# Kernel optimization log

Measured on AMD Instinct MI355X. Metric: run time of the kernel, lower is better.

## Reference

```python
import jax, jax.numpy as jnp
import numpy as np

DIM = 1024
NUM_HEADS = 16
HEAD_DIM = DIM // NUM_HEADS
WINDOW = 128
EPS = 1e-5


def setup_inputs() -> dict:
    key = jax.random.key(0)
    ks = jax.random.split(key, 8)
    B, S, D = 1, 2048, DIM
    x = jax.random.normal(ks[0], (B, S, D), dtype=jnp.float32)
    # xavier-uniform-ish scale for linear weights (torch layout: [out, in])
    def xavier(k, out_f, in_f):
        lim = np.sqrt(6.0 / (in_f + out_f)).astype(np.float32)
        return jax.random.uniform(k, (out_f, in_f), jnp.float32, -lim, lim)
    qkv_w = xavier(ks[1], 3 * D, D)
    out_w = xavier(ks[2], D, D)
    ln_g = jnp.ones((D,), jnp.float32)
    ln_b = jnp.zeros((D,), jnp.float32)
    w1 = xavier(ks[3], 4 * D, D)
    b1 = jnp.zeros((4 * D,), jnp.float32)
    w2 = xavier(ks[4], D, 4 * D)
    b2 = jnp.zeros((D,), jnp.float32)
    return {"x": x, "qkv_w": qkv_w, "out_w": out_w, "ln_g": ln_g,
            "ln_b": ln_b, "w1": w1, "b1": b1, "w2": w2, "b2": b2}


def reference(x, qkv_w, out_w, ln_g, ln_b, w1, b1, w2, b2):
    B, S, D = x.shape
    H, hd = NUM_HEADS, HEAD_DIM
    residual = x
    # LayerNorm (pre-norm)
    mu = jnp.mean(x, axis=-1, keepdims=True)
    var = jnp.var(x, axis=-1, keepdims=True)
    xn = (x - mu) * jax.lax.rsqrt(var + EPS) * ln_g + ln_b
    # QKV projection (torch Linear: y = x @ W^T)
    qkv = xn @ qkv_w.T                              # [B,S,3D]
    qkv = qkv.reshape(B, S, 3, H, hd).transpose(2, 0, 3, 1, 4)  # [3,B,H,S,hd]
    q, k, v = qkv[0], qkv[1], qkv[2]
    # Local-window boolean mask: |i - j| <= window_size // 2
    w = WINDOW // 2
    i = jnp.arange(S)[:, None]
    j = jnp.arange(S)[None, :]
    local_mask = jnp.abs(i - j) <= w                # [S,S]
    # SDPA with boolean mask
    scale = 1.0 / np.sqrt(hd).astype(np.float32)
    scores = jnp.einsum('bhqd,bhkd->bhqk', q, k) * scale
    scores = jnp.where(local_mask, scores, -jnp.inf)
    attn = jax.nn.softmax(scores, axis=-1)
    attn_out = jnp.einsum('bhqk,bhkd->bhqd', attn, v)
    attn_out = attn_out.transpose(0, 2, 1, 3).reshape(B, S, D)
    attn_out = attn_out @ out_w.T
    out = residual + attn_out
    # FFN (no second norm in this module), exact GELU
    h = jax.nn.gelu(out @ w1.T + b1, approximate=False)
    ffn_out = h @ w2.T + b2
    return out + ffn_out
```

## Files before the change

kernel.cpp:

```cpp
#include <hip/hip_runtime.h>
#include <math.h>

typedef unsigned short u16;
typedef __attribute__((ext_vector_type(8))) short short8;
typedef __attribute__((ext_vector_type(4))) float f32x4;
typedef __attribute__((ext_vector_type(4))) int i32x4;
typedef __attribute__((ext_vector_type(4))) u16 u16x4;

#define AS1 __attribute__((address_space(1)))
#define AS3 __attribute__((address_space(3)))

__device__ inline u16 f2bf(float f){
  union { float f; unsigned int u; } x; x.f = f;
  unsigned int r = x.u + 0x7fffu + ((x.u >> 16) & 1u);
  return (u16)(r >> 16);
}
__device__ inline float bf2f(u16 u){
  union { unsigned int u; float f; } x; x.u = ((unsigned int)u) << 16;
  return x.f;
}
__device__ inline float gelu_fast(float v){
  float y = 0.7978845608f * (v + 0.044715f * v * v * v);
  float e = __expf(2.0f * y);
  return v - v / (e + 1.0f);
}

__global__ __launch_bounds__(256) void prep_kernel(
    const float* __restrict__ x, const float* __restrict__ g, const float* __restrict__ b,
    u16* __restrict__ xn,
    const float* __restrict__ qkv_w, u16* __restrict__ qkvw_b,
    const float* __restrict__ out_w, u16* __restrict__ outw_b,
    const float* __restrict__ w1,    u16* __restrict__ w1_b,
    const float* __restrict__ w2,    u16* __restrict__ w2_b)
{
  const int tid = threadIdx.x;
  int bid = blockIdx.x;
  if (bid < 2048){
    const int row = bid;
    float4 v = *(const float4*)(x + (size_t)row*1024 + tid*4);
    float s  = v.x + v.y + v.z + v.w;
    float ss = v.x*v.x + v.y*v.y + v.z*v.z + v.w*v.w;
    #pragma unroll
    for (int off = 32; off; off >>= 1){
      s  += __shfl_xor(s,  off, 64);
      ss += __shfl_xor(ss, off, 64);
    }
    __shared__ float red[8];
    const int wid = tid >> 6;
    if ((tid & 63) == 0){ red[wid] = s; red[4+wid] = ss; }
    __syncthreads();
    float S  = red[0]+red[1]+red[2]+red[3];
    float SS = red[4]+red[5]+red[6]+red[7];
    float mu  = S * (1.0f/1024.0f);
    float var = SS * (1.0f/1024.0f) - mu*mu;
    float rs  = rsqrtf(var + 1e-5f);
    float4 gv = *(const float4*)(g + tid*4);
    float4 bv = *(const float4*)(b + tid*4);
    u16x4 pk;
    pk.x = f2bf((v.x-mu)*rs*gv.x + bv.x);
    pk.y = f2bf((v.y-mu)*rs*gv.y + bv.y);
    pk.z = f2bf((v.z-mu)*rs*gv.z + bv.z);
    pk.w = f2bf((v.w-mu)*rs*gv.w + bv.w);
    *(u16x4*)(xn + (size_t)row*1024 + tid*4) = pk;
    return;
  }
  bid -= 2048;
  const float* src; u16* dst;
  if (bid < 3072){ src = qkv_w; dst = qkvw_b; }
  else if (bid < 3072+1024){ src = out_w; dst = outw_b; bid -= 3072; }
  else if (bid < 3072+1024+4096){ src = w1; dst = w1_b; bid -= 3072+1024; }
  else { src = w2; dst = w2_b; bid -= 3072+1024+4096; }
  const size_t i = ((size_t)bid*256 + tid) * 4;
  float4 v = *(const float4*)(src + i);
  u16x4 pk;
  pk.x = f2bf(v.x); pk.y = f2bf(v.y); pk.z = f2bf(v.z); pk.w = f2bf(v.w);
  *(u16x4*)(dst + i) = pk;
}

template<int EPI, int BM, int BN, int WAVES>
__global__ __launch_bounds__(WAVES*64) void gemm_lds(
    const u16* __restrict__ A, const u16* __restrict__ B,
    float* __restrict__ outF, u16* __restrict__ outB,
    const float* __restrict__ bias, const float* __restrict__ resid,
    int M, int N, int K, int nbx, int nwg, int Kc)
{
  constexpr int WR  = (WAVES == 8) ? 4 : 2;
  constexpr int WC  = 2;
  constexpr int MI  = BM / WR / 16;
  constexpr int NJ  = BN / WC / 16;
  constexpr int ACH = BM / 8 / WAVES;
  constexpr int BCH = BN / 8 / WAVES;
  __shared__ u16 As[2][BM*64];
  __shared__ u16 Bs[2][BN*64];
  const int tid = threadIdx.x;
  const int l   = tid & 63;
  const int w   = tid >> 6;
  const int wr  = w & (WR-1), wc = w / WR;
  const int orig = blockIdx.x;
  const int wgid = (orig & 7) * (nwg >> 3) + (orig >> 3);
  const int bcol = wgid % nbx, brow = wgid / nbx;
  const int kz = blockIdx.y;
  const int l15 = l & 15, l4 = l >> 4;

  const u16* Ab = A + (size_t)brow*BM*K + (size_t)kz*Kc;
  const u16* Bb = B + (size_t)bcol*BN*K + (size_t)kz*Kc;

  f32x4 acc[MI][NJ];
  #pragma unroll
  for (int i = 0; i < MI; ++i)
    #pragma unroll
    for (int j = 0; j < NJ; ++j)
      acc[i][j] = (f32x4){0.f, 0.f, 0.f, 0.f};

  const int rsub = l >> 3;
  const int csrc = ((l & 7) ^ rsub) * 8;
  const int swz  = (l15 & 7) * 8;
  const int nkt = Kc >> 6;

  auto stage = [&](int kt, int buf){
    const u16* Ag = Ab + kt*64 + csrc;
    const u16* Bg = Bb + kt*64 + csrc;
    #pragma unroll
    for (int i = 0; i < ACH; ++i){
      const int ca = w*ACH + i;
      __builtin_amdgcn_global_load_lds(
        (const AS1 void*)(Ag + (size_t)(ca*8 + rsub)*K),
        (AS3 void*)(&As[buf][ca*512]), 16, 0, 0);
    }
    #pragma unroll
    for (int i = 0; i < BCH; ++i){
      const int cb = w*BCH + i;
      __builtin_amdgcn_global_load_lds(
        (const AS1 void*)(Bg + (size_t)(cb*8 + rsub)*K),
        (AS3 void*)(&Bs[buf][cb*512]), 16, 0, 0);
    }
  };

  stage(0, 0);
  __syncthreads();
  for (int kt = 0; kt < nkt; ++kt){
    const int cur = kt & 1;
    if (kt + 1 < nkt) stage(kt + 1, cur ^ 1);
    #pragma unroll
    for (int ks = 0; ks < 2; ++ks){
      const int kop = (ks*32 + l4*8) ^ swz;
      short8 af[MI], bfr[NJ];
      #pragma unroll
      for (int i = 0; i < MI; ++i)
        af[i]  = *(const short8*)&As[cur][(wr*(BM/WR) + i*16 + l15)*64 + kop];
      #pragma unroll
      for (int j = 0; j < NJ; ++j)
        bfr[j] = *(const short8*)&Bs[cur][(wc*(BN/WC) + j*16 + l15)*64 + kop];
      #pragma unroll
      for (int i = 0; i < MI; ++i)
        #pragma unroll
        for (int j = 0; j < NJ; ++j)
          acc[i][j] = __builtin_amdgcn_mfma_f32_16x16x32_bf16(af[i], bfr[j], acc[i][j], 0, 0, 0);
    }
    __syncthreads();
  }

  #pragma unroll
  for (int i = 0; i < MI; ++i){
    #pragma unroll
    for (int j = 0; j < NJ; ++j){
      #pragma unroll
      for (int r = 0; r < 4; ++r){
        int row = brow*BM + wr*(BM/WR) + i*16 + l4*4 + r;
        int col = bcol*BN + wc*(BN/WC) + j*16 + l15;
        float v = acc[i][j][r];
        size_t o = (size_t)row * N + col;
        if constexpr (EPI == 0){
          outB[o] = f2bf(v);
        } else if constexpr (EPI == 1){
          v += resid[o];
          outB[o] = f2bf(v);
        } else if constexpr (EPI == 2){
          v += bias[col];
          outB[o] = f2bf(gelu_fast(v));
        } else {
          outB[(size_t)kz * M * N + o] = f2bf(v);
        }
      }
    }
  }
}

__global__ __launch_bounds__(256) void reduce_ffn2(const u16* __restrict__ p,
                                                   const float* __restrict__ bias,
                                                   const u16* __restrict__ resid_b,
                                                   float* __restrict__ out){
  const size_t s = (size_t)2048*1024;
  const size_t i = ((size_t)blockIdx.x * 256 + threadIdx.x) * 4;
  u16x4 a0 = *(const u16x4*)(p + i);
  u16x4 a1 = *(const u16x4*)(p + s + i);
  u16x4 a2 = *(const u16x4*)(p + 2*s + i);
  u16x4 a3 = *(const u16x4*)(p + 3*s + i);
  u16x4 rb = *(const u16x4*)(resid_b + i);
  float4 bb = *(const float4*)(bias + (i & 1023));
  float4 o;
  o.x = bf2f(a0.x) + bf2f(a1.x) + bf2f(a2.x) + bf2f(a3.x) + bf2f(rb.x) + bb.x;
  o.y = bf2f(a0.y) + bf2f(a1.y) + bf2f(a2.y) + bf2f(a3.y) + bf2f(rb.y) + bb.y;
  o.z = bf2f(a0.z) + bf2f(a1.z) + bf2f(a2.z) + bf2f(a3.z) + bf2f(rb.z) + bb.z;
  o.w = bf2f(a0.w) + bf2f(a1.w) + bf2f(a2.w) + bf2f(a3.w) + bf2f(rb.w) + bb.w;
  *(float4*)(out + i) = o;
}

__global__ __launch_bounds__(256) void attn_kernel(const u16* __restrict__ qkv, u16* __restrict__ attn_out){
  constexpr int S = 2048, D3 = 3072;
  const int qt = blockIdx.x, h = blockIdx.y;
  const int q0 = qt * 64;
  const int tid = threadIdx.x;
  const int l = tid & 63, w = tid >> 6;
  const int l15 = l & 15, l4 = l >> 4;

  __shared__ u16 smem[29696];
  u16 (*Qs)[72]  = (u16(*)[72]) (smem);
  u16 *Ks        = smem + 4608;
  u16 (*Ps)[200] = (u16(*)[200])(smem);
  u16 (*Vt)[200] = (u16(*)[200])(smem + 16896);

  #pragma unroll
  for (int i = 0; i < 2; ++i){
    int cid = tid + 256*i; int r = cid >> 3, c = cid & 7;
    *(i32x4*)&Qs[r][c*8] = *(const i32x4*)(qkv + (size_t)(q0 + r)*D3 + h*64 + c*8);
  }
  {
    const int rsubK = l >> 3;
    const int csrcK = ((l & 7) ^ rsubK) * 8;
    #pragma unroll
    for (int i = 0; i < 6; ++i){
      const int ca = w*6 + i;
      const long kj = (long)(q0 - 64 + ca*8 + rsubK);
      __builtin_amdgcn_global_load_lds(
        (const AS1 void*)(qkv + kj*D3 + 1024 + h*64 + csrcK),
        (AS3 void*)(Ks + ca*512), 16, 0, 0);
    }
  }
  #pragma unroll
  for (int i = 0; i < 6; ++i){
    int cid = tid + 256*i; int r = cid >> 3, c = cid & 7;
    int kj = q0 - 64 + r;
    i32x4 vv = {0,0,0,0};
    if (kj >= 0 && kj < S)
      vv = *(const i32x4*)(qkv + (size_t)kj*D3 + 2048 + h*64 + c*8);
    union { i32x4 v; u16 u[8]; } uu; uu.v = vv;
    #pragma unroll
    for (int j = 0; j < 8; ++j) Vt[c*8 + j][r] = uu.u[j];
  }
  __syncthreads();

  f32x4 sc[12];
  #pragma unroll
  for (int cf = 0; cf < 12; ++cf) sc[cf] = (f32x4){0.f,0.f,0.f,0.f};
  const int ko = l4 * 8;
  const int swzK = (l15 & 7) * 8;
  short8 a0 = *(const short8*)&Qs[16*w + l15][ko];
  short8 a1 = *(const short8*)&Qs[16*w + l15][32 + ko];
  #pragma unroll
  for (int cf = 0; cf < 12; ++cf){
    short8 b0 = *(const short8*)&Ks[(cf*16 + l15)*64 + (ko ^ swzK)];
    short8 b1 = *(const short8*)&Ks[(cf*16 + l15)*64 + ((32 + ko) ^ swzK)];
    sc[cf] = __builtin_amdgcn_mfma_f32_16x16x32_bf16(a0, b0, sc[cf], 0, 0, 0);
    sc[cf] = __builtin_amdgcn_mfma_f32_16x16x32_bf16(a1, b1, sc[cf], 0, 0, 0);
  }
  __syncthreads();

  const float scale = 0.125f;
  #pragma unroll
  for (int r = 0; r < 4; ++r){
    const int qrl = 16*w + l4*4 + r;
    float mx = -1e30f;
    #pragma unroll
    for (int cf = 0; cf < 12; ++cf){
      int j  = cf*16 + l15;
      int kj = q0 - 64 + j;
      bool ok = (j >= qrl) && (j <= qrl + 128) && (kj >= 0) && (kj < S);
      float sv = ok ? sc[cf][r]*scale : -1e30f;
      sc[cf][r] = sv;
      mx = fmaxf(mx, sv);
    }
    #pragma unroll
    for (int off = 1; off < 16; off <<= 1) mx = fmaxf(mx, __shfl_xor(mx, off, 64));
    float sm = 0.f;
    #pragma unroll
    for (int cf = 0; cf < 12; ++cf){
      float pv = __expf(sc[cf][r] - mx);
      sc[cf][r] = pv;
      sm += pv;
    }
    #pragma unroll
    for (int off = 1; off < 16; off <<= 1) sm += __shfl_xor(sm, off, 64);
    float inv = 1.0f / sm;
    #pragma unroll
    for (int cf = 0; cf < 12; ++cf) Ps[qrl][cf*16 + l15] = f2bf(sc[cf][r] * inv);
  }
  __syncthreads();

  f32x4 o[4];
  #pragma unroll
  for (int df = 0; df < 4; ++df) o[df] = (f32x4){0.f,0.f,0.f,0.f};
  #pragma unroll
  for (int kk = 0; kk < 6; ++kk){
    short8 a = *(const short8*)&Ps[16*w + l15][kk*32 + ko];
    #pragma unroll
    for (int df = 0; df < 4; ++df){
      short8 b = *(const short8*)&Vt[df*16 + l15][kk*32 + ko];
      o[df] = __builtin_amdgcn_mfma_f32_16x16x32_bf16(a, b, o[df], 0, 0, 0);
    }
  }
  #pragma unroll
  for (int df = 0; df < 4; ++df){
    #pragma unroll
    for (int r = 0; r < 4; ++r){
      attn_out[(size_t)(q0 + 16*w + l4*4 + r)*1024 + h*64 + df*16 + l15] = f2bf(o[df][r]);
    }
  }
}

extern "C" void kernel_launch(void* const* d_in, const int* in_sizes, int n_in,
                              void* d_out, int out_size, void* d_ws, size_t ws_size,
                              hipStream_t stream)
{
  const float* x     = (const float*)d_in[0];
  const float* qkv_w = (const float*)d_in[1];
  const float* out_w = (const float*)d_in[2];
  const float* ln_g  = (const float*)d_in[3];
  const float* ln_b  = (const float*)d_in[4];
  const float* w1    = (const float*)d_in[5];
  const float* b1    = (const float*)d_in[6];
  const float* w2    = (const float*)d_in[7];
  const float* b2    = (const float*)d_in[8];
  float* out_final = (float*)d_out;

  char* p = (char*)d_ws;
  u16* xn_b   = (u16*)p; p += (size_t)2048*1024*2;
  u16* qkv_b  = (u16*)p; p += (size_t)2048*3072*2;
  u16* attn_b = (u16*)p; p += (size_t)2048*1024*2;
  u16* out_b  = (u16*)p; p += (size_t)2048*1024*2;
  u16* qkvw_b = (u16*)p; p += (size_t)3072*1024*2;
  u16* outw_b = (u16*)p; p += (size_t)1024*1024*2;
  u16* w1_b   = (u16*)p; p += (size_t)4096*1024*2;
  u16* w2_b   = (u16*)p; p += (size_t)1024*4096*2;
  u16* h_b    = (u16*)p; p += (size_t)2048*4096*2;
  u16* partials = (u16*)p;

  prep_kernel<<<14336, 256, 0, stream>>>(x, ln_g, ln_b, xn_b,
                                         qkv_w, qkvw_b, out_w, outw_b,
                                         w1, w1_b, w2, w2_b);
  gemm_lds<0,128,64,8><<<dim3(768), 512, 0, stream>>>(xn_b, qkvw_b, nullptr, qkv_b, nullptr, nullptr,
                                                      2048, 3072, 1024, 48, 768, 1024);
  attn_kernel<<<dim3(32,16), 256, 0, stream>>>(qkv_b, attn_b);
  gemm_lds<1,64,64,4><<<dim3(512), 256, 0, stream>>>(attn_b, outw_b, nullptr, out_b, nullptr, x,
                                                     2048, 1024, 1024, 16, 512, 1024);
  gemm_lds<2,128,128,8><<<dim3(512), 512, 0, stream>>>(out_b, w1_b, nullptr, h_b, b1, nullptr,
                                                       2048, 4096, 1024, 32, 512, 1024);
  gemm_lds<4,128,128,8><<<dim3(128, 4), 512, 0, stream>>>(h_b, w2_b, nullptr, partials, nullptr, nullptr,
                                                          2048, 1024, 4096, 8, 128, 1024);
  reduce_ffn2<<<2048, 256, 0, stream>>>(partials, b2, out_b, out_final);
}
```

Baseline: 117.0 us.

## Fuse bias/residual into FFN2 split-K epilogue, swizzle attention P, widen reduce

Moves the b2 bias and residual add into the kz==0 split-K partial of the FFN2 GEMM, so the reduce kernel only sums four partials and uses 8-wide loads. The attention kernel now loads Q straight into registers instead of staging it through LDS, and stores P with an XOR swizzle to cut LDS bank conflicts, which also shrinks shared memory. The out-projection GEMM launch goes from 4 to 8 waves at the same tile size. The trade-off is that the bias and residual are now rounded to bf16 together with the partial, adding a little precision loss.

```diff
diff --git a/kernel.cpp b/kernel.cpp
--- a/kernel.cpp
+++ b/kernel.cpp
@@ -82,6 +82,7 @@
     const u16* __restrict__ A, const u16* __restrict__ B,
     float* __restrict__ outF, u16* __restrict__ outB,
     const float* __restrict__ bias, const float* __restrict__ resid,
+    const u16* __restrict__ residB,
     int M, int N, int K, int nbx, int nwg, int Kc)
 {
   constexpr int WR  = (WAVES == 8) ? 4 : 2;
@@ -179,6 +180,7 @@
           v += bias[col];
           outB[o] = f2bf(gelu_fast(v));
         } else {
+          if (kz == 0) v += bias[col] + bf2f(residB[o]);
           outB[(size_t)kz * M * N + o] = f2bf(v);
         }
       }
@@ -187,23 +189,19 @@
 }
 
 __global__ __launch_bounds__(256) void reduce_ffn2(const u16* __restrict__ p,
-                                                   const float* __restrict__ bias,
-                                                   const u16* __restrict__ resid_b,
                                                    float* __restrict__ out){
   const size_t s = (size_t)2048*1024;
-  const size_t i = ((size_t)blockIdx.x * 256 + threadIdx.x) * 4;
-  u16x4 a0 = *(const u16x4*)(p + i);
-  u16x4 a1 = *(const u16x4*)(p + s + i);
-  u16x4 a2 = *(const u16x4*)(p + 2*s + i);
-  u16x4 a3 = *(const u16x4*)(p + 3*s + i);
-  u16x4 rb = *(const u16x4*)(resid_b + i);
-  float4 bb = *(const float4*)(bias + (i & 1023));
-  float4 o;
-  o.x = bf2f(a0.x) + bf2f(a1.x) + bf2f(a2.x) + bf2f(a3.x) + bf2f(rb.x) + bb.x;
-  o.y = bf2f(a0.y) + bf2f(a1.y) + bf2f(a2.y) + bf2f(a3.y) + bf2f(rb.y) + bb.y;
-  o.z = bf2f(a0.z) + bf2f(a1.z) + bf2f(a2.z) + bf2f(a3.z) + bf2f(rb.z) + bb.z;
-  o.w = bf2f(a0.w) + bf2f(a1.w) + bf2f(a2.w) + bf2f(a3.w) + bf2f(rb.w) + bb.w;
-  *(float4*)(out + i) = o;
+  const size_t i = ((size_t)blockIdx.x * 256 + threadIdx.x) * 8;
+  short8 a0 = *(const short8*)(p + i);
+  short8 a1 = *(const short8*)(p + s + i);
+  short8 a2 = *(const short8*)(p + 2*s + i);
+  short8 a3 = *(const short8*)(p + 3*s + i);
+  float o[8];
+  #pragma unroll
+  for (int j = 0; j < 8; ++j)
+    o[j] = bf2f((u16)a0[j]) + bf2f((u16)a1[j]) + bf2f((u16)a2[j]) + bf2f((u16)a3[j]);
+  *(float4*)(out + i)     = (float4){o[0], o[1], o[2], o[3]};
+  *(float4*)(out + i + 4) = (float4){o[4], o[5], o[6], o[7]};
 }
 
 __global__ __launch_bounds__(256) void attn_kernel(const u16* __restrict__ qkv, u16* __restrict__ attn_out){
@@ -214,17 +212,15 @@
   const int l = tid & 63, w = tid >> 6;
   const int l15 = l & 15, l4 = l >> 4;
 
-  __shared__ u16 smem[29696];
-  u16 (*Qs)[72]  = (u16(*)[72]) (smem);
-  u16 *Ks        = smem + 4608;
-  u16 (*Ps)[200] = (u16(*)[200])(smem);
-  u16 (*Vt)[200] = (u16(*)[200])(smem + 16896);
-
-  #pragma unroll
-  for (int i = 0; i < 2; ++i){
-    int cid = tid + 256*i; int r = cid >> 3, c = cid & 7;
-    *(i32x4*)&Qs[r][c*8] = *(const i32x4*)(qkv + (size_t)(q0 + r)*D3 + h*64 + c*8);
-  }
+  __shared__ u16 smem[24832];
+  u16 *Ks = smem;
+  u16 (*Vt)[196] = (u16(*)[196])(smem + 12288);
+  char* Pb = (char*)smem;
+
+  const u16* qrow = qkv + (size_t)(q0 + 16*w + l15)*D3 + h*64;
+  short8 a0 = *(const short8*)(qrow + l4*8);
+  short8 a1 = *(const short8*)(qrow + 32 + l4*8);
+
   {
     const int rsubK = l >> 3;
     const int csrcK = ((l & 7) ^ rsubK) * 8;
@@ -255,8 +251,6 @@
   for (int cf = 0; cf < 12; ++cf) sc[cf] = (f32x4){0.f,0.f,0.f,0.f};
   const int ko = l4 * 8;
   const int swzK = (l15 & 7) * 8;
-  short8 a0 = *(const short8*)&Qs[16*w + l15][ko];
-  short8 a1 = *(const short8*)&Qs[16*w + l15][32 + ko];
   #pragma unroll
   for (int cf = 0; cf < 12; ++cf){
     short8 b0 = *(const short8*)&Ks[(cf*16 + l15)*64 + (ko ^ swzK)];
@@ -293,16 +287,21 @@
     for (int off = 1; off < 16; off <<= 1) sm += __shfl_xor(sm, off, 64);
     float inv = 1.0f / sm;
     #pragma unroll
-    for (int cf = 0; cf < 12; ++cf) Ps[qrl][cf*16 + l15] = f2bf(sc[cf][r] * inv);
+    for (int cf = 0; cf < 12; ++cf){
+      unsigned off = (unsigned)(qrl*384 + (cf*16 + l15)*2);
+      *(u16*)(Pb + (off ^ (unsigned)((qrl & 7) << 4))) = f2bf(sc[cf][r] * inv);
+    }
   }
   __syncthreads();
 
   f32x4 o[4];
   #pragma unroll
   for (int df = 0; df < 4; ++df) o[df] = (f32x4){0.f,0.f,0.f,0.f};
+  const unsigned pswz = (unsigned)((l15 & 7) << 4);
   #pragma unroll
   for (int kk = 0; kk < 6; ++kk){
-    short8 a = *(const short8*)&Ps[16*w + l15][kk*32 + ko];
+    unsigned off = (unsigned)((16*w + l15)*384 + (kk*32 + ko)*2);
+    short8 a = *(const short8*)(Pb + (off ^ pswz));
     #pragma unroll
     for (int df = 0; df < 4; ++df){
       short8 b = *(const short8*)&Vt[df*16 + l15][kk*32 + ko];
@@ -348,14 +347,14 @@
   prep_kernel<<<14336, 256, 0, stream>>>(x, ln_g, ln_b, xn_b,
                                          qkv_w, qkvw_b, out_w, outw_b,
                                          w1, w1_b, w2, w2_b);
-  gemm_lds<0,128,64,8><<<dim3(768), 512, 0, stream>>>(xn_b, qkvw_b, nullptr, qkv_b, nullptr, nullptr,
+  gemm_lds<0,128,64,8><<<dim3(768), 512, 0, stream>>>(xn_b, qkvw_b, nullptr, qkv_b, nullptr, nullptr, nullptr,
                                                       2048, 3072, 1024, 48, 768, 1024);
   attn_kernel<<<dim3(32,16), 256, 0, stream>>>(qkv_b, attn_b);
-  gemm_lds<1,64,64,4><<<dim3(512), 256, 0, stream>>>(attn_b, outw_b, nullptr, out_b, nullptr, x,
+  gemm_lds<1,64,64,8><<<dim3(512), 512, 0, stream>>>(attn_b, outw_b, nullptr, out_b, nullptr, x, nullptr,
                                                      2048, 1024, 1024, 16, 512, 1024);
-  gemm_lds<2,128,128,8><<<dim3(512), 512, 0, stream>>>(out_b, w1_b, nullptr, h_b, b1, nullptr,
+  gemm_lds<2,128,128,8><<<dim3(512), 512, 0, stream>>>(out_b, w1_b, nullptr, h_b, b1, nullptr, nullptr,
                                                        2048, 4096, 1024, 32, 512, 1024);
-  gemm_lds<4,128,128,8><<<dim3(128, 4), 512, 0, stream>>>(h_b, w2_b, nullptr, partials, nullptr, nullptr,
+  gemm_lds<4,128,128,8><<<dim3(128, 4), 512, 0, stream>>>(h_b, w2_b, nullptr, partials, b2, nullptr, out_b,
                                                           2048, 1024, 4096, 8, 128, 1024);
-  reduce_ffn2<<<2048, 256, 0, stream>>>(partials, b2, out_b, out_final);
-}
+  reduce_ffn2<<<1024, 256, 0, stream>>>(partials, out_final);
+}
```

After: 123.7 us. +5.7%, slower.
